# Performance work log

Hardware: AMD Instinct MI355X
Metric: run time of the kernel (lower is better)

## Reference

```python
import jax, jax.numpy as jnp
import numpy as np

ROPE_BASE = 10000.0
NEG_INF = jnp.finfo(jnp.float32).min


def _rope(x, pos):
    # x: [B, L, H, D], pos: [L] absolute positions. Rotate-half RoPE.
    D = x.shape[-1]
    half = D // 2
    inv_freq = 1.0 / (ROPE_BASE ** (jnp.arange(half, dtype=jnp.float32) / half))
    ang = pos.astype(jnp.float32)[:, None] * inv_freq  # [L, half]
    cos = jnp.cos(ang)[None, :, None, :]
    sin = jnp.sin(ang)[None, :, None, :]
    x1, x2 = x[..., :half], x[..., half:]
    return jnp.concatenate([x1 * cos - x2 * sin, x1 * sin + x2 * cos], axis=-1)


def setup_inputs() -> dict:
    key = jax.random.key(0)
    kq, kk, kv = jax.random.split(key, 3)
    B, L, H, Dh = 4, 4096, 16, 64
    return {
        "q": jax.random.normal(kq, (B, L, H, Dh), dtype=jnp.float32),
        "k": jax.random.normal(kk, (B, L, H, Dh), dtype=jnp.float32),
        "v": jax.random.normal(kv, (B, L, H, Dh), dtype=jnp.float32),
        "chunk_size": 1024,
        "start_index": 0,
    }


def reference(q, k, v, chunk_size, start_index):
    B, L, H, Dh = q.shape
    Dv = v.shape[-1]
    C = chunk_size
    assert L % C == 0  # chosen shapes avoid padding; original pads otherwise
    n = L // C
    # Per-chunk RoPE with offset start_index + chunk_offset equals
    # full-sequence RoPE at absolute positions start_index + arange(L).
    pos = start_index + jnp.arange(L)
    q_rot = _rope(q.astype(jnp.float32), pos)
    k_rot = _rope(k.astype(jnp.float32), pos)
    qc = q_rot.reshape(B, n, C, H, Dh)
    kc = k_rot.reshape(B, n, C, H, Dh)
    vc = v.astype(jnp.float32).reshape(B, n, C, H, Dv)
    # Unscaled (scale=1.0) block-diagonal causal attention.
    scores = jnp.einsum("bnqhd,bnkhd->bnhqk", qc, kc)
    causal = jnp.tril(jnp.ones((C, C), dtype=jnp.bool_))
    scores = jnp.where(causal, scores, NEG_INF)
    attn = jax.nn.softmax(scores, axis=-1)
    attn = jnp.where(jnp.isnan(attn), 0.0, attn)
    out = jnp.einsum("bnhqk,bnkhd->bnqhd", attn, vc)
    return out.reshape(B, L, H, Dv).astype(q.dtype)
```

## Files before the change

### kernel.cpp

```cpp
#include <hip/hip_runtime.h>

typedef _Float16 f16x8 __attribute__((ext_vector_type(8)));
typedef _Float16 f16x4 __attribute__((ext_vector_type(4)));
typedef float    f32x4 __attribute__((ext_vector_type(4)));

#define B_N    4
#define L_TOT  4096
#define H_N    16
#define DH     64
#define HALF_D 32
#define QT     64
#define KT     64
#define LDSP   72

#define LOG2_BASE 13.287712379549449f

#define TAB_BYTES  ((size_t)L_TOT * 64 * sizeof(float))
#define IMG_BYTES  ((size_t)B_N * H_N * 64 * 8192)

__global__ void rope_table_kernel(const int* __restrict__ sidx, float* __restrict__ tab) {
    int idx = blockIdx.x * 256 + (int)threadIdx.x;
    if (idx >= L_TOT * HALF_D) return;
    int l = idx >> 5;
    int j = idx & 31;
    float invf = exp2f(-(float)j * (LOG2_BASE / (float)HALF_D));
    float ang = (float)(sidx[0] + l) * invf;
    float s, c;
    sincosf(ang, &s, &c);
    tab[l * 64 + j] = c;
    tab[l * 64 + HALF_D + j] = s;
}

__global__ __launch_bounds__(256)
void kprep_kernel(const float* __restrict__ k, const float* __restrict__ tab,
                  unsigned char* __restrict__ kimg) {
    int task = blockIdx.x * 256 + (int)threadIdx.x;
    int c = task & 7;
    int rowid = task >> 3;
    int l = rowid & (L_TOT - 1);
    int bh = rowid >> 12;
    int b = bh >> 4, h = bh & 15;
    int d0 = c * 8;
    const float* src = k + (((size_t)b * L_TOT + l) * H_N + h) * (size_t)DH;
    f32x4 xo0 = *(const f32x4*)(src + d0);
    f32x4 xo1 = *(const f32x4*)(src + d0 + 4);
    int dp = d0 ^ 32;
    f32x4 xp0 = *(const f32x4*)(src + dp);
    f32x4 xp1 = *(const f32x4*)(src + dp + 4);
    int dm = d0 & 31;
    const float* tr = tab + (size_t)l * 64;
    f32x4 c0 = *(const f32x4*)(tr + dm);
    f32x4 c1 = *(const f32x4*)(tr + dm + 4);
    f32x4 s0 = *(const f32x4*)(tr + 32 + dm);
    f32x4 s1 = *(const f32x4*)(tr + 32 + dm + 4);
    float sgn = (d0 < 32) ? -1.f : 1.f;
    f16x8 o;
#pragma unroll
    for (int j = 0; j < 4; ++j) {
        o[j]     = (_Float16)(xo0[j] * c0[j] + sgn * xp0[j] * s0[j]);
        o[j + 4] = (_Float16)(xo1[j] * c1[j] + sgn * xp1[j] * s1[j]);
    }
    size_t tile = (size_t)bh * 64 + (l >> 6);
    unsigned char* dst = kimg + tile * 8192 + (size_t)(l & 63) * 128 + ((c ^ (l & 7)) << 4);
    *(f16x8*)dst = o;
}

__global__ __launch_bounds__(256)
void vprep_kernel(const float* __restrict__ v, unsigned char* __restrict__ vimg) {
    __shared__ float Vs[64][65];
    int bid = blockIdx.x;
    int tile = bid & 63;
    int h = (bid >> 6) & 15;
    int b = bid >> 10;
    int kbase = tile * 64;
    int t = (int)threadIdx.x;
    int row = t >> 2, cb = t & 3;
    const float* src = v + (((size_t)b * L_TOT + kbase + row) * H_N + h) * (size_t)DH + cb * 16;
    f32x4 a0 = *(const f32x4*)(src);
    f32x4 a1 = *(const f32x4*)(src + 4);
    f32x4 a2 = *(const f32x4*)(src + 8);
    f32x4 a3 = *(const f32x4*)(src + 12);
#pragma unroll
    for (int j = 0; j < 4; ++j) {
        Vs[row][cb * 16 + j]      = a0[j];
        Vs[row][cb * 16 + 4 + j]  = a1[j];
        Vs[row][cb * 16 + 8 + j]  = a2[j];
        Vs[row][cb * 16 + 12 + j] = a3[j];
    }
    __syncthreads();
    size_t tbase = ((size_t)(b * 16 + h) * 64 + tile) * 8192;
#pragma unroll
    for (int e = 0; e < 2; ++e) {
        int task = e * 256 + t;
        int dv = task >> 3, c = task & 7;
        f16x8 o;
#pragma unroll
        for (int j = 0; j < 8; ++j) o[j] = (_Float16)Vs[8 * c + j][dv];
        unsigned char* dst = vimg + tbase + (size_t)dv * 128 + ((c ^ (dv & 7)) << 4);
        *(f16x8*)dst = o;
    }
}

__device__ __forceinline__ void gl_lds16(const void* g, void* lds) {
    __builtin_amdgcn_global_load_lds(
        (const __attribute__((address_space(1))) unsigned int*)g,
        (__attribute__((address_space(3))) unsigned int*)lds, 16, 0, 0);
}

__global__ __launch_bounds__(256)
void attn_main_kernel(const float* __restrict__ q, const int* __restrict__ csz,
                      const float* __restrict__ tab,
                      const unsigned char* __restrict__ kimg,
                      const unsigned char* __restrict__ vimg,
                      float* __restrict__ out) {
    __shared__ __align__(16) unsigned char smem[40960];

    const int tid  = (int)threadIdx.x;
    const int lane = tid & 63;
    const int w    = tid >> 6;
    const int cl   = lane & 15;
    const int g    = lane >> 4;
    const int e7   = cl & 7;

    const int bid0  = (int)blockIdx.x;
    const int wg    = (bid0 & 7) * 512 + (bid0 >> 3);
    const int qtile = wg & 63;
    const int h     = (wg >> 6) & 15;
    const int b     = wg >> 10;

    const int C   = csz[0];
    const int tpc = C >> 6;
    const int kb0 = (qtile / tpc) * tpc;

    const int qr = qtile * QT + w * 16 + cl;
    const float* qs = q + (((size_t)b * L_TOT + qr) * H_N + h) * (size_t)DH;
    f32x4 x1a = *(const f32x4*)(qs + 8 * g);
    f32x4 x1b = *(const f32x4*)(qs + 8 * g + 4);
    f32x4 x2a = *(const f32x4*)(qs + 8 * g + HALF_D);
    f32x4 x2b = *(const f32x4*)(qs + 8 * g + HALF_D + 4);
    const float* tr = tab + (size_t)qr * 64 + 8 * g;
    f32x4 ca = *(const f32x4*)(tr);
    f32x4 cb = *(const f32x4*)(tr + 4);
    f32x4 sa = *(const f32x4*)(tr + HALF_D);
    f32x4 sb = *(const f32x4*)(tr + HALF_D + 4);
    f16x8 qa0, qa1;
#pragma unroll
    for (int j = 0; j < 4; ++j) {
        qa0[j]     = (_Float16)(x1a[j] * ca[j] - x2a[j] * sa[j]);
        qa0[j + 4] = (_Float16)(x1b[j] * cb[j] - x2b[j] * sb[j]);
        qa1[j]     = (_Float16)(x1a[j] * sa[j] + x2a[j] * ca[j]);
        qa1[j + 4] = (_Float16)(x1b[j] * sb[j] + x2b[j] * cb[j]);
    }

    const unsigned char* ksrc = kimg + (size_t)(b * 16 + h) * 64 * 8192;
    const unsigned char* vsrc = vimg + (size_t)(b * 16 + h) * 64 * 8192;

    f32x4 o[4] = {};
    float m = -3e38f, l = 0.f;

    {
#pragma unroll
        for (int i = 0; i < 4; ++i) {
            int off = w * 4096 + i * 1024;
            const unsigned char* gs = (off < 8192)
                ? ksrc + (size_t)kb0 * 8192 + off
                : vsrc + (size_t)kb0 * 8192 + (off - 8192);
            gl_lds16(gs + lane * 16, smem + off);
        }
    }
    asm volatile("s_waitcnt vmcnt(0)");
    __syncthreads();

    int pb = 0;
    for (int kb = kb0; kb <= qtile; ++kb) {
        if (kb < qtile) {
#pragma unroll
            for (int i = 0; i < 4; ++i) {
                int off = w * 4096 + i * 1024;
                const unsigned char* gs = (off < 8192)
                    ? ksrc + (size_t)(kb + 1) * 8192 + off
                    : vsrc + (size_t)(kb + 1) * 8192 + (off - 8192);
                gl_lds16(gs + lane * 16, smem + (pb ^ 1) * 16384 + off);
            }
        }

        const char* Kb = (const char*)(smem + pb * 16384);
        const char* Vb = (const char*)(smem + pb * 16384 + 8192);

        f32x4 sc[4];
#pragma unroll
        for (int ct = 0; ct < 4; ++ct) {
            int rb = (ct * 16 + cl) * 128;
            f16x8 kf0 = *(const f16x8*)(Kb + rb + ((g ^ e7) << 4));
            f16x8 kf1 = *(const f16x8*)(Kb + rb + (((g + 4) ^ e7) << 4));
            f32x4 z = {};
            z = __builtin_amdgcn_mfma_f32_16x16x32_f16(kf0, qa0, z, 0, 0, 0);
            sc[ct] = __builtin_amdgcn_mfma_f32_16x16x32_f16(kf1, qa1, z, 0, 0, 0);
        }

        if (kb == qtile) {
            const int qloc = w * 16 + cl;
#pragma unroll
            for (int ct = 0; ct < 4; ++ct)
#pragma unroll
                for (int r = 0; r < 4; ++r)
                    if (ct * 16 + 4 * g + r > qloc) sc[ct][r] = -3e38f;
        }

        float mx = sc[0][0];
#pragma unroll
        for (int ct = 0; ct < 4; ++ct)
#pragma unroll
            for (int r = 0; r < 4; ++r) mx = fmaxf(mx, sc[ct][r]);
        mx = fmaxf(mx, __shfl_xor(mx, 16));
        mx = fmaxf(mx, __shfl_xor(mx, 32));
        float mn  = fmaxf(m, mx);
        float scl = __expf(m - mn);
        m = mn;
        float ps = 0.f;
#pragma unroll
        for (int ct = 0; ct < 4; ++ct)
#pragma unroll
            for (int r = 0; r < 4; ++r) {
                float p = __expf(sc[ct][r] - mn);
                sc[ct][r] = p;
                ps += p;
            }
        ps += __shfl_xor(ps, 16);
        ps += __shfl_xor(ps, 32);
        l = l * scl + ps;
#pragma unroll
        for (int ct = 0; ct < 4; ++ct)
#pragma unroll
            for (int r = 0; r < 4; ++r) o[ct][r] *= scl;

        char* Pw = (char*)(smem + 32768 + w * 2048);
#pragma unroll
        for (int c = 0; c < 4; ++c) {
            int chunk = (2 * c + (g >> 1)) ^ e7;
            f16x4 pv;
#pragma unroll
            for (int r = 0; r < 4; ++r) pv[r] = (_Float16)sc[c][r];
            *(f16x4*)(Pw + cl * 128 + (chunk << 4) + (g & 1) * 8) = pv;
        }

#pragma unroll
        for (int st = 0; st < 2; ++st) {
            f16x8 pa = *(const f16x8*)(Pw + cl * 128 + (((4 * st + g) ^ e7) << 4));
#pragma unroll
            for (int ct = 0; ct < 4; ++ct) {
                f16x8 vb = *(const f16x8*)(Vb + (ct * 16 + cl) * 128 + (((4 * st + g) ^ e7) << 4));
                o[ct] = __builtin_amdgcn_mfma_f32_16x16x32_f16(vb, pa, o[ct], 0, 0, 0);
            }
        }

        asm volatile("s_waitcnt vmcnt(0)");
        __syncthreads();
        pb ^= 1;
    }

    float* Ow = (float*)smem;
    float inv = 1.f / l;
#pragma unroll
    for (int ct = 0; ct < 4; ++ct)
#pragma unroll
        for (int r = 0; r < 4; ++r)
            Ow[(w * 16 + cl) * 66 + ct * 16 + 4 * g + r] = o[ct][r] * inv;
    __syncthreads();
    int row_l = tid >> 2;
    int cb4 = (tid & 3) * 16;
    const float* orow = Ow + row_l * 66 + cb4;
    float* gdst = out + (((size_t)b * L_TOT + qtile * QT + row_l) * H_N + h) * (size_t)DH + cb4;
#pragma unroll
    for (int jj = 0; jj < 4; ++jj) {
        f32x4 val;
#pragma unroll
        for (int x = 0; x < 4; ++x) val[x] = orow[4 * jj + x];
        *(f32x4*)(gdst + 4 * jj) = val;
    }
}

__device__ __forceinline__ void rope_cs_inline(float pos, int d, float* cc, float* ss) {
    float invf = exp2f(-(float)d * (LOG2_BASE / (float)HALF_D));
    float s, c;
    sincosf(pos * invf, &s, &c);
    *cc = c;
    *ss = s;
}

template<bool TAB>
__global__ __launch_bounds__(256)
void chunked_attn_kernel(const float* __restrict__ q, const float* __restrict__ k,
                         const float* __restrict__ v, const int* __restrict__ csz,
                         const int* __restrict__ sidx, const float* __restrict__ tab,
                         float* __restrict__ out)
{
    __shared__ _Float16 Ks[KT][LDSP];
    __shared__ _Float16 Vt[DH][LDSP];
    __shared__ _Float16 Ps[4][16][LDSP];

    const int tid  = (int)threadIdx.x;
    const int lane = tid & 63;
    const int w    = tid >> 6;
    const int cl   = lane & 15;
    const int g    = lane >> 4;

    const int bid   = (int)blockIdx.x;
    const int qtile = bid & (L_TOT / QT - 1);
    const int h     = (bid >> 6) & (H_N - 1);
    const int b     = bid >> 10;

    const int C   = csz[0];
    const int S0  = sidx[0];
    const int tpc = C / KT;
    const int kb0 = (qtile / tpc) * tpc;

    const int qrow = qtile * QT + w * 16 + cl;
    const size_t qoff = (((size_t)b * L_TOT + qrow) * H_N + h) * (size_t)DH;
    f32x4 x1a = *(const f32x4*)(q + qoff + 8 * g);
    f32x4 x1b = *(const f32x4*)(q + qoff + 8 * g + 4);
    f32x4 x2a = *(const f32x4*)(q + qoff + 8 * g + HALF_D);
    f32x4 x2b = *(const f32x4*)(q + qoff + 8 * g + HALF_D + 4);
    f32x4 ca, cb, sa, sb;
    if (TAB) {
        const float* tr = tab + (size_t)qrow * 64 + 8 * g;
        ca = *(const f32x4*)(tr);
        cb = *(const f32x4*)(tr + 4);
        sa = *(const f32x4*)(tr + HALF_D);
        sb = *(const f32x4*)(tr + HALF_D + 4);
    } else {
        float pos = (float)(S0 + qrow);
#pragma unroll
        for (int j = 0; j < 4; ++j) {
            float c0, s0, c1, s1;
            rope_cs_inline(pos, 8 * g + j,     &c0, &s0);
            rope_cs_inline(pos, 8 * g + 4 + j, &c1, &s1);
            ca[j] = c0; sa[j] = s0;
            cb[j] = c1; sb[j] = s1;
        }
    }
    f16x8 qa0, qa1;
#pragma unroll
    for (int j = 0; j < 4; ++j) {
        qa0[j]     = (_Float16)(x1a[j] * ca[j] - x2a[j] * sa[j]);
        qa0[j + 4] = (_Float16)(x1b[j] * cb[j] - x2b[j] * sb[j]);
        qa1[j]     = (_Float16)(x1a[j] * sa[j] + x2a[j] * ca[j]);
        qa1[j + 4] = (_Float16)(x1b[j] * sb[j] + x2b[j] * cb[j]);
    }

    f32x4 o[4] = {};
    float m_r[4], l_r[4];
#pragma unroll
    for (int r = 0; r < 4; ++r) { m_r[r] = -3e38f; l_r[r] = 0.f; }

    for (int kb = kb0; kb <= qtile; ++kb) {
        __syncthreads();
        const int kbase = kb * KT;

#pragma unroll
        for (int e = 0; e < 2; ++e) {
            int task = e * 256 + tid;
            int kk = task >> 3;
            int dg = (task & 7) * 4;
            int grow = kbase + kk;
            size_t off = (((size_t)b * L_TOT + grow) * H_N + h) * (size_t)DH;
            f32x4 x1 = *(const f32x4*)(k + off + dg);
            f32x4 x2 = *(const f32x4*)(k + off + dg + HALF_D);
            f32x4 cc, ss;
            if (TAB) {
                const float* tr2 = tab + (size_t)grow * 64 + dg;
                cc = *(const f32x4*)(tr2);
                ss = *(const f32x4*)(tr2 + HALF_D);
            } else {
                float pos = (float)(S0 + grow);
#pragma unroll
                for (int j = 0; j < 4; ++j) {
                    float c0, s0;
                    rope_cs_inline(pos, dg + j, &c0, &s0);
                    cc[j] = c0; ss[j] = s0;
                }
            }
            f16x4 o1, o2;
#pragma unroll
            for (int j = 0; j < 4; ++j) {
                o1[j] = (_Float16)(x1[j] * cc[j] - x2[j] * ss[j]);
                o2[j] = (_Float16)(x1[j] * ss[j] + x2[j] * cc[j]);
            }
            *(f16x4*)&Ks[kk][dg]          = o1;
            *(f16x4*)&Ks[kk][dg + HALF_D] = o2;
        }

#pragma unroll
        for (int e = 0; e < 4; ++e) {
            int task = e * 256 + tid;
            int kk = task >> 4;
            int dq = (task & 15) * 4;
            int grow = kbase + kk;
            size_t off = (((size_t)b * L_TOT + grow) * H_N + h) * (size_t)DH + dq;
            f32x4 x = *(const f32x4*)(v + off);
#pragma unroll
            for (int i = 0; i < 4; ++i) Vt[dq + i][kk] = (_Float16)x[i];
        }
        __syncthreads();

        f32x4 sc[4];
#pragma unroll
        for (int ct = 0; ct < 4; ++ct) {
            f16x8 kf0 = *(const f16x8*)&Ks[ct * 16 + cl][8 * g];
            f16x8 kf1 = *(const f16x8*)&Ks[ct * 16 + cl][8 * g + HALF_D];
            f32x4 z = {};
            z = __builtin_amdgcn_mfma_f32_16x16x32_f16(qa0, kf0, z, 0, 0, 0);
            sc[ct] = __builtin_amdgcn_mfma_f32_16x16x32_f16(qa1, kf1, z, 0, 0, 0);
        }

        const int rowt = w * 16 + 4 * g;
        if (kb == qtile) {
#pragma unroll
            for (int ct = 0; ct < 4; ++ct)
#pragma unroll
                for (int r = 0; r < 4; ++r)
                    if (ct * 16 + cl > rowt + r) sc[ct][r] = -3e38f;
        }

        f32x4 mt;
#pragma unroll
        for (int r = 0; r < 4; ++r)
            mt[r] = fmaxf(fmaxf(sc[0][r], sc[1][r]), fmaxf(sc[2][r], sc[3][r]));
#pragma unroll
        for (int off = 1; off < 16; off <<= 1) {
#pragma unroll
            for (int r = 0; r < 4; ++r)
                mt[r] = fmaxf(mt[r], __shfl_xor(mt[r], off));
        }
        float scale_r[4];
#pragma unroll
        for (int r = 0; r < 4; ++r) {
            float mn = fmaxf(m_r[r], mt[r]);
            scale_r[r] = __expf(m_r[r] - mn);
            m_r[r] = mn;
        }
        f32x4 psum = {};
#pragma unroll
        for (int ct = 0; ct < 4; ++ct) {
#pragma unroll
            for (int r = 0; r < 4; ++r) {
                float p = __expf(sc[ct][r] - m_r[r]);
                sc[ct][r] = p;
                psum[r] += p;
            }
        }
#pragma unroll
        for (int off = 1; off < 16; off <<= 1) {
#pragma unroll
            for (int r = 0; r < 4; ++r)
                psum[r] += __shfl_xor(psum[r], off);
        }
#pragma unroll
        for (int r = 0; r < 4; ++r) l_r[r] = l_r[r] * scale_r[r] + psum[r];
#pragma unroll
        for (int ct = 0; ct < 4; ++ct)
#pragma unroll
            for (int r = 0; r < 4; ++r) o[ct][r] *= scale_r[r];

#pragma unroll
        for (int ct = 0; ct < 4; ++ct)
#pragma unroll
            for (int r = 0; r < 4; ++r)
                Ps[w][4 * g + r][ct * 16 + cl] = (_Float16)sc[ct][r];

#pragma unroll
        for (int st = 0; st < 2; ++st) {
            f16x8 pa = *(const f16x8*)&Ps[w][cl][8 * g + 32 * st];
#pragma unroll
            for (int ct = 0; ct < 4; ++ct) {
                f16x8 vb = *(const f16x8*)&Vt[ct * 16 + cl][8 * g + 32 * st];
                o[ct] = __builtin_amdgcn_mfma_f32_16x16x32_f16(pa, vb, o[ct], 0, 0, 0);
            }
        }
    }

#pragma unroll
    for (int ct = 0; ct < 4; ++ct) {
#pragma unroll
        for (int r = 0; r < 4; ++r) {
            int row = qtile * QT + w * 16 + 4 * g + r;
            float val = o[ct][r] / l_r[r];
            out[(((size_t)b * L_TOT + row) * H_N + h) * (size_t)DH + ct * 16 + cl] = val;
        }
    }
}

extern "C" void kernel_launch(void* const* d_in, const int* in_sizes, int n_in,
                              void* d_out, int out_size, void* d_ws, size_t ws_size,
                              hipStream_t stream) {
    const float* q  = (const float*)d_in[0];
    const float* k  = (const float*)d_in[1];
    const float* v  = (const float*)d_in[2];
    const int* csz  = (const int*)d_in[3];
    const int* sidx = (const int*)d_in[4];
    float* out = (float*)d_out;

    const size_t TOTAL = TAB_BYTES + 2 * IMG_BYTES;
    const int grid = B_N * H_N * (L_TOT / QT);

    if (ws_size >= TOTAL) {
        float* tab = (float*)d_ws;
        unsigned char* kimg = (unsigned char*)d_ws + TAB_BYTES;
        unsigned char* vimg = kimg + IMG_BYTES;
        rope_table_kernel<<<(L_TOT * HALF_D + 255) / 256, 256, 0, stream>>>(sidx, tab);
        kprep_kernel<<<B_N * H_N * L_TOT * 8 / 256, 256, 0, stream>>>(k, tab, kimg);
        vprep_kernel<<<B_N * H_N * 64, 256, 0, stream>>>(v, vimg);
        attn_main_kernel<<<grid, 256, 0, stream>>>(q, csz, tab, kimg, vimg, out);
    } else if (ws_size >= TAB_BYTES) {
        float* tab = (float*)d_ws;
        rope_table_kernel<<<(L_TOT * HALF_D + 255) / 256, 256, 0, stream>>>(sidx, tab);
        chunked_attn_kernel<true><<<grid, 256, 0, stream>>>(q, k, v, csz, sidx, tab, out);
    } else {
        chunked_attn_kernel<false><<<grid, 256, 0, stream>>>(q, k, v, csz, sidx, nullptr, out);
    }
}
```

Baseline: 153.9 us.

## Merge K/V prep kernels, stream V from global, add lazy softmax rescale

```diff
diff --git a/kernel.cpp b/kernel.cpp
--- a/kernel.cpp
+++ b/kernel.cpp
@@ -2,6 +2,7 @@
 
 typedef _Float16 f16x8 __attribute__((ext_vector_type(8)));
 typedef _Float16 f16x4 __attribute__((ext_vector_type(4)));
+typedef _Float16 f16x2 __attribute__((ext_vector_type(2)));
 typedef float    f32x4 __attribute__((ext_vector_type(4)));
 
 #define B_N    4
@@ -14,6 +15,7 @@
 #define LDSP   72
 
 #define LOG2_BASE 13.287712379549449f
+#define LOG2E     1.4426950408889634f
 
 #define TAB_BYTES  ((size_t)L_TOT * 64 * sizeof(float))
 #define IMG_BYTES  ((size_t)B_N * H_N * 64 * 8192)
@@ -32,72 +34,75 @@
 }
 
 __global__ __launch_bounds__(256)
-void kprep_kernel(const float* __restrict__ k, const float* __restrict__ tab,
-                  unsigned char* __restrict__ kimg) {
-    int task = blockIdx.x * 256 + (int)threadIdx.x;
-    int c = task & 7;
-    int rowid = task >> 3;
-    int l = rowid & (L_TOT - 1);
-    int bh = rowid >> 12;
-    int b = bh >> 4, h = bh & 15;
-    int d0 = c * 8;
-    const float* src = k + (((size_t)b * L_TOT + l) * H_N + h) * (size_t)DH;
-    f32x4 xo0 = *(const f32x4*)(src + d0);
-    f32x4 xo1 = *(const f32x4*)(src + d0 + 4);
-    int dp = d0 ^ 32;
-    f32x4 xp0 = *(const f32x4*)(src + dp);
-    f32x4 xp1 = *(const f32x4*)(src + dp + 4);
-    int dm = d0 & 31;
-    const float* tr = tab + (size_t)l * 64;
-    f32x4 c0 = *(const f32x4*)(tr + dm);
-    f32x4 c1 = *(const f32x4*)(tr + dm + 4);
-    f32x4 s0 = *(const f32x4*)(tr + 32 + dm);
-    f32x4 s1 = *(const f32x4*)(tr + 32 + dm + 4);
-    float sgn = (d0 < 32) ? -1.f : 1.f;
-    f16x8 o;
-#pragma unroll
-    for (int j = 0; j < 4; ++j) {
-        o[j]     = (_Float16)(xo0[j] * c0[j] + sgn * xp0[j] * s0[j]);
-        o[j + 4] = (_Float16)(xo1[j] * c1[j] + sgn * xp1[j] * s1[j]);
-    }
-    size_t tile = (size_t)bh * 64 + (l >> 6);
-    unsigned char* dst = kimg + tile * 8192 + (size_t)(l & 63) * 128 + ((c ^ (l & 7)) << 4);
-    *(f16x8*)dst = o;
-}
-
-__global__ __launch_bounds__(256)
-void vprep_kernel(const float* __restrict__ v, unsigned char* __restrict__ vimg) {
+void prep_kernel(const float* __restrict__ k, const float* __restrict__ v,
+                 const float* __restrict__ tab,
+                 unsigned char* __restrict__ kimg, unsigned char* __restrict__ vimg)
+{
     __shared__ float Vs[64][65];
-    int bid = blockIdx.x;
-    int tile = bid & 63;
-    int h = (bid >> 6) & 15;
-    int b = bid >> 10;
-    int kbase = tile * 64;
+    int bid = (int)blockIdx.x;
     int t = (int)threadIdx.x;
-    int row = t >> 2, cb = t & 3;
-    const float* src = v + (((size_t)b * L_TOT + kbase + row) * H_N + h) * (size_t)DH + cb * 16;
-    f32x4 a0 = *(const f32x4*)(src);
-    f32x4 a1 = *(const f32x4*)(src + 4);
-    f32x4 a2 = *(const f32x4*)(src + 8);
-    f32x4 a3 = *(const f32x4*)(src + 12);
-#pragma unroll
-    for (int j = 0; j < 4; ++j) {
-        Vs[row][cb * 16 + j]      = a0[j];
-        Vs[row][cb * 16 + 4 + j]  = a1[j];
-        Vs[row][cb * 16 + 8 + j]  = a2[j];
-        Vs[row][cb * 16 + 12 + j] = a3[j];
-    }
-    __syncthreads();
-    size_t tbase = ((size_t)(b * 16 + h) * 64 + tile) * 8192;
-#pragma unroll
-    for (int e = 0; e < 2; ++e) {
-        int task = e * 256 + t;
-        int dv = task >> 3, c = task & 7;
-        f16x8 o;
-#pragma unroll
-        for (int j = 0; j < 8; ++j) o[j] = (_Float16)Vs[8 * c + j][dv];
-        unsigned char* dst = vimg + tbase + (size_t)dv * 128 + ((c ^ (dv & 7)) << 4);
-        *(f16x8*)dst = o;
+
+    if (bid < 4096) {
+        int task = bid * 256 + t;
+        int c = task & 3;
+        int rowid = task >> 2;
+        int l = rowid & (L_TOT - 1);
+        int bh = rowid >> 12;
+        int b = bh >> 4, h = bh & 15;
+        int d0 = c * 8;
+        const float* src = k + (((size_t)b * L_TOT + l) * H_N + h) * (size_t)DH;
+        f32x4 x1a = *(const f32x4*)(src + d0);
+        f32x4 x1b = *(const f32x4*)(src + d0 + 4);
+        f32x4 x2a = *(const f32x4*)(src + d0 + HALF_D);
+        f32x4 x2b = *(const f32x4*)(src + d0 + HALF_D + 4);
+        const float* tr = tab + (size_t)l * 64 + d0;
+        f32x4 ca = *(const f32x4*)(tr);
+        f32x4 cb = *(const f32x4*)(tr + 4);
+        f32x4 sa = *(const f32x4*)(tr + HALF_D);
+        f32x4 sb = *(const f32x4*)(tr + HALF_D + 4);
+        f16x8 olo, ohi;
+#pragma unroll
+        for (int j = 0; j < 4; ++j) {
+            olo[j]     = (_Float16)(x1a[j] * ca[j] - x2a[j] * sa[j]);
+            olo[j + 4] = (_Float16)(x1b[j] * cb[j] - x2b[j] * sb[j]);
+            ohi[j]     = (_Float16)(x1a[j] * sa[j] + x2a[j] * ca[j]);
+            ohi[j + 4] = (_Float16)(x1b[j] * sb[j] + x2b[j] * cb[j]);
+        }
+        size_t tile = (size_t)bh * 64 + (l >> 6);
+        unsigned char* dst = kimg + tile * 8192 + (size_t)(l & 63) * 128;
+        int sw = (c ^ (l & 7)) << 4;
+        *(f16x8*)(dst + sw)        = olo;
+        *(f16x8*)(dst + (sw ^ 64)) = ohi;
+    } else {
+        int vb = bid - 4096;
+        int tile = vb & 63;
+        int h = (vb >> 6) & 15;
+        int b = vb >> 10;
+        int kbase = tile * 64;
+        int row = t >> 2, cb = t & 3;
+        const float* src = v + (((size_t)b * L_TOT + kbase + row) * H_N + h) * (size_t)DH + cb * 16;
+        f32x4 a0 = *(const f32x4*)(src);
+        f32x4 a1 = *(const f32x4*)(src + 4);
+        f32x4 a2 = *(const f32x4*)(src + 8);
+        f32x4 a3 = *(const f32x4*)(src + 12);
+#pragma unroll
+        for (int j = 0; j < 4; ++j) {
+            Vs[row][cb * 16 + j]      = a0[j];
+            Vs[row][cb * 16 + 4 + j]  = a1[j];
+            Vs[row][cb * 16 + 8 + j]  = a2[j];
+            Vs[row][cb * 16 + 12 + j] = a3[j];
+        }
+        __syncthreads();
+        size_t tbase = ((size_t)(b * 16 + h) * 64 + tile) * 8192;
+#pragma unroll
+        for (int e = 0; e < 2; ++e) {
+            int task = e * 256 + t;
+            int dv = task >> 3, c = task & 7;
+            f16x8 o;
+#pragma unroll
+            for (int j = 0; j < 8; ++j) o[j] = (_Float16)Vs[8 * c + j][dv];
+            *(f16x8*)(vimg + tbase + (size_t)dv * 128 + (c << 4)) = o;
+        }
     }
 }
 
@@ -107,13 +112,13 @@
         (__attribute__((address_space(3))) unsigned int*)lds, 16, 0, 0);
 }
 
-__global__ __launch_bounds__(256)
+__global__ __launch_bounds__(256, 6)
 void attn_main_kernel(const float* __restrict__ q, const int* __restrict__ csz,
                       const float* __restrict__ tab,
                       const unsigned char* __restrict__ kimg,
                       const unsigned char* __restrict__ vimg,
                       float* __restrict__ out) {
-    __shared__ __align__(16) unsigned char smem[40960];
+    __shared__ __align__(16) unsigned char smem[24576];
 
     const int tid  = (int)threadIdx.x;
     const int lane = tid & 63;
@@ -124,12 +129,13 @@
 
     const int bid0  = (int)blockIdx.x;
     const int wg    = (bid0 & 7) * 512 + (bid0 >> 3);
-    const int qtile = wg & 63;
+    const int qx    = wg & 63;
     const int h     = (wg >> 6) & 15;
     const int b     = wg >> 10;
 
     const int C   = csz[0];
     const int tpc = C >> 6;
+    const int qtile = qx ^ ((tpc - 1) & 63);
     const int kb0 = (qtile / tpc) * tpc;
 
     const int qr = qtile * QT + w * 16 + cl;
@@ -146,57 +152,58 @@
     f16x8 qa0, qa1;
 #pragma unroll
     for (int j = 0; j < 4; ++j) {
-        qa0[j]     = (_Float16)(x1a[j] * ca[j] - x2a[j] * sa[j]);
-        qa0[j + 4] = (_Float16)(x1b[j] * cb[j] - x2b[j] * sb[j]);
-        qa1[j]     = (_Float16)(x1a[j] * sa[j] + x2a[j] * ca[j]);
-        qa1[j + 4] = (_Float16)(x1b[j] * sb[j] + x2b[j] * cb[j]);
+        qa0[j]     = (_Float16)((x1a[j] * ca[j] - x2a[j] * sa[j]) * LOG2E);
+        qa0[j + 4] = (_Float16)((x1b[j] * cb[j] - x2b[j] * sb[j]) * LOG2E);
+        qa1[j]     = (_Float16)((x1a[j] * sa[j] + x2a[j] * ca[j]) * LOG2E);
+        qa1[j + 4] = (_Float16)((x1b[j] * sb[j] + x2b[j] * cb[j]) * LOG2E);
     }
 
     const unsigned char* ksrc = kimg + (size_t)(b * 16 + h) * 64 * 8192;
     const unsigned char* vsrc = vimg + (size_t)(b * 16 + h) * 64 * 8192;
 
+    const int krd  = cl * 128 + ((g ^ e7) << 4);
+    const int pwb  = cl * 128 + (((g >> 1) ^ e7) << 4) + (g & 1) * 8;
+    const int vln  = cl * 128 + g * 16;
+    char* Pw = (char*)(smem + 16384 + w * 2048);
+
     f32x4 o[4] = {};
     float m = -3e38f, l = 0.f;
 
     {
-#pragma unroll
-        for (int i = 0; i < 4; ++i) {
-            int off = w * 4096 + i * 1024;
-            const unsigned char* gs = (off < 8192)
-                ? ksrc + (size_t)kb0 * 8192 + off
-                : vsrc + (size_t)kb0 * 8192 + (off - 8192);
-            gl_lds16(gs + lane * 16, smem + off);
-        }
-    }
-    asm volatile("s_waitcnt vmcnt(0)");
-    __syncthreads();
+        const unsigned char* gs = ksrc + (size_t)kb0 * 8192;
+        gl_lds16(gs + tid * 16, smem + tid * 16);
+        gl_lds16(gs + tid * 16 + 4096, smem + tid * 16 + 4096);
+    }
 
     int pb = 0;
     for (int kb = kb0; kb <= qtile; ++kb) {
+        __syncthreads();
+
+        const char* Kb = (const char*)(smem + pb * 8192);
         if (kb < qtile) {
-#pragma unroll
-            for (int i = 0; i < 4; ++i) {
-                int off = w * 4096 + i * 1024;
-                const unsigned char* gs = (off < 8192)
-                    ? ksrc + (size_t)(kb + 1) * 8192 + off
-                    : vsrc + (size_t)(kb + 1) * 8192 + (off - 8192);
-                gl_lds16(gs + lane * 16, smem + (pb ^ 1) * 16384 + off);
-            }
-        }
-
-        const char* Kb = (const char*)(smem + pb * 16384);
-        const char* Vb = (const char*)(smem + pb * 16384 + 8192);
+            const unsigned char* gs = ksrc + (size_t)(kb + 1) * 8192;
+            unsigned char* ld = smem + (pb ^ 1) * 8192;
+            gl_lds16(gs + tid * 16, ld + tid * 16);
+            gl_lds16(gs + tid * 16 + 4096, ld + tid * 16 + 4096);
+        }
 
         f32x4 sc[4];
+        __builtin_amdgcn_s_setprio(1);
 #pragma unroll
         for (int ct = 0; ct < 4; ++ct) {
-            int rb = (ct * 16 + cl) * 128;
-            f16x8 kf0 = *(const f16x8*)(Kb + rb + ((g ^ e7) << 4));
-            f16x8 kf1 = *(const f16x8*)(Kb + rb + (((g + 4) ^ e7) << 4));
+            const char* kr = Kb + krd + ct * 2048;
+            f16x8 kf0 = *(const f16x8*)(kr);
+            f16x8 kf1 = *(const f16x8*)(Kb + ((krd + ct * 2048) ^ 64));
             f32x4 z = {};
             z = __builtin_amdgcn_mfma_f32_16x16x32_f16(kf0, qa0, z, 0, 0, 0);
             sc[ct] = __builtin_amdgcn_mfma_f32_16x16x32_f16(kf1, qa1, z, 0, 0, 0);
         }
+        __builtin_amdgcn_s_setprio(0);
+
+        const unsigned char* vtile = vsrc + (size_t)kb * 8192;
+        f16x8 va[4];
+#pragma unroll
+        for (int ct = 0; ct < 4; ++ct) va[ct] = *(const f16x8*)(vtile + vln + ct * 2048);
 
         if (kb == qtile) {
             const int qloc = w * 16 + cl;
@@ -214,51 +221,56 @@
             for (int r = 0; r < 4; ++r) mx = fmaxf(mx, sc[ct][r]);
         mx = fmaxf(mx, __shfl_xor(mx, 16));
         mx = fmaxf(mx, __shfl_xor(mx, 32));
-        float mn  = fmaxf(m, mx);
-        float scl = __expf(m - mn);
-        m = mn;
+        if (__any(mx - m > 8.0f)) {
+            float mn  = fmaxf(m, mx);
+            float scl = exp2f(m - mn);
+            m = mn;
+            l *= scl;
+#pragma unroll
+            for (int ct = 0; ct < 4; ++ct)
+#pragma unroll
+                for (int r = 0; r < 4; ++r) o[ct][r] *= scl;
+        }
         float ps = 0.f;
 #pragma unroll
         for (int ct = 0; ct < 4; ++ct)
 #pragma unroll
             for (int r = 0; r < 4; ++r) {
-                float p = __expf(sc[ct][r] - mn);
+                float p = exp2f(sc[ct][r] - m);
                 sc[ct][r] = p;
                 ps += p;
             }
         ps += __shfl_xor(ps, 16);
         ps += __shfl_xor(ps, 32);
-        l = l * scl + ps;
+        l += ps;
+
+#pragma unroll
+        for (int c = 0; c < 4; ++c) {
+            f16x2 lo = __builtin_bit_cast(f16x2, __builtin_amdgcn_cvt_pkrtz(sc[c][0], sc[c][1]));
+            f16x2 hi = __builtin_bit_cast(f16x2, __builtin_amdgcn_cvt_pkrtz(sc[c][2], sc[c][3]));
+            f16x4 pv = __builtin_shufflevector(lo, hi, 0, 1, 2, 3);
+            *(f16x4*)(Pw + (pwb ^ (c << 5))) = pv;
+        }
+
+        f16x8 vbb[4];
+#pragma unroll
+        for (int ct = 0; ct < 4; ++ct) vbb[ct] = *(const f16x8*)(vtile + vln + ct * 2048 + 64);
+
+        f16x8 pa0 = *(const f16x8*)(Pw + krd);
+        f16x8 pa1 = *(const f16x8*)(Pw + (krd ^ 64));
+        __builtin_amdgcn_s_setprio(1);
 #pragma unroll
         for (int ct = 0; ct < 4; ++ct)
-#pragma unroll
-            for (int r = 0; r < 4; ++r) o[ct][r] *= scl;
-
-        char* Pw = (char*)(smem + 32768 + w * 2048);
-#pragma unroll
-        for (int c = 0; c < 4; ++c) {
-            int chunk = (2 * c + (g >> 1)) ^ e7;
-            f16x4 pv;
-#pragma unroll
-            for (int r = 0; r < 4; ++r) pv[r] = (_Float16)sc[c][r];
-            *(f16x4*)(Pw + cl * 128 + (chunk << 4) + (g & 1) * 8) = pv;
-        }
-
-#pragma unroll
-        for (int st = 0; st < 2; ++st) {
-            f16x8 pa = *(const f16x8*)(Pw + cl * 128 + (((4 * st + g) ^ e7) << 4));
-#pragma unroll
-            for (int ct = 0; ct < 4; ++ct) {
-                f16x8 vb = *(const f16x8*)(Vb + (ct * 16 + cl) * 128 + (((4 * st + g) ^ e7) << 4));
-                o[ct] = __builtin_amdgcn_mfma_f32_16x16x32_f16(vb, pa, o[ct], 0, 0, 0);
-            }
-        }
-
-        asm volatile("s_waitcnt vmcnt(0)");
-        __syncthreads();
+            o[ct] = __builtin_amdgcn_mfma_f32_16x16x32_f16(va[ct], pa0, o[ct], 0, 0, 0);
+#pragma unroll
+        for (int ct = 0; ct < 4; ++ct)
+            o[ct] = __builtin_amdgcn_mfma_f32_16x16x32_f16(vbb[ct], pa1, o[ct], 0, 0, 0);
+        __builtin_amdgcn_s_setprio(0);
+
         pb ^= 1;
     }
 
+    __syncthreads();
     float* Ow = (float*)smem;
     float inv = 1.f / l;
 #pragma unroll
@@ -508,8 +520,7 @@
         unsigned char* kimg = (unsigned char*)d_ws + TAB_BYTES;
         unsigned char* vimg = kimg + IMG_BYTES;
         rope_table_kernel<<<(L_TOT * HALF_D + 255) / 256, 256, 0, stream>>>(sidx, tab);
-        kprep_kernel<<<B_N * H_N * L_TOT * 8 / 256, 256, 0, stream>>>(k, tab, kimg);
-        vprep_kernel<<<B_N * H_N * 64, 256, 0, stream>>>(v, vimg);
+        prep_kernel<<<8192, 256, 0, stream>>>(k, v, tab, kimg, vimg);
         attn_main_kernel<<<grid, 256, 0, stream>>>(q, csz, tab, kimg, vimg, out);
     } else if (ws_size >= TAB_BYTES) {
         float* tab = (float*)d_ws;
```

Result: slower. 310.5 us (+101.8%).
